# Kernel optimization log

Hardware: AMD Instinct MI355X
Metric: run time of the kernel (lower is better)

## Reference

```python
import jax, jax.numpy as jnp
import numpy as np

N = 3000          # num_sample (nodes)
N_OMICS = 3000    # input feature dims for both omics
ENC1, ENC2, NZ = 256, 128, 64


def _xavier(key, fan_in, fan_out):
    limit = float(np.sqrt(6.0 / (fan_in + fan_out)))
    return jax.random.uniform(key, (fan_in, fan_out), jnp.float32, -limit, limit)


def setup_inputs() -> dict:
    key = jax.random.key(0)
    ks = jax.random.split(key, 20)
    inp = {
        "omics_1": jax.random.normal(ks[0], (N, N_OMICS), jnp.float32),
        "omics_2": jax.random.normal(ks[1], (N, N_OMICS), jnp.float32),
    }
    # random dense adjacency, row-normalized (as a typical normalized graph operator)
    for i, name in enumerate(["adj_feature_omics1", "adj_feature_omics2",
                              "adj_spatial_omics1", "adj_spatial_omics2"]):
        a = jax.random.uniform(ks[2 + i], (N, N), jnp.float32)
        inp[name] = a / jnp.sum(a, axis=1, keepdims=True)
    # GNNLayer weights for the four GAE encoders (xavier uniform, as in reset_parameters)
    dims = [(N_OMICS, ENC1), (ENC1, ENC2), (ENC2, NZ)]
    kidx = 6
    for enc in ["f1", "f2", "s1", "s2"]:
        for li, (fi, fo) in enumerate(dims, start=1):
            inp[f"w_{enc}_{li}"] = _xavier(ks[kidx], fi, fo)
            kidx += 1
    return inp


def _gae_encoder(x, adj, w1, w2, w3):
    # GNNLayer: support = act(x @ W); out = spmm(adj, support). Dropout is identity (eval).
    z = adj @ jnp.tanh(x @ w1)          # [N, ENC1]
    z = adj @ jnp.tanh(z @ w2)          # [N, ENC2]
    z = adj @ (z @ w3)                  # [N, NZ]  (no activation on layer 3)
    adj_hat = jax.nn.sigmoid(z @ z.T)   # [N, N]
    return z, adj_hat


def reference(omics_1, omics_2,
              adj_feature_omics1, adj_feature_omics2,
              adj_spatial_omics1, adj_spatial_omics2,
              w_f1_1, w_f1_2, w_f1_3,
              w_f2_1, w_f2_2, w_f2_3,
              w_s1_1, w_s1_2, w_s1_3,
              w_s2_1, w_s2_2, w_s2_3):
    _, a1 = _gae_encoder(omics_1, adj_feature_omics1, w_f1_1, w_f1_2, w_f1_3)
    _, a2 = _gae_encoder(omics_2, adj_feature_omics2, w_f2_1, w_f2_2, w_f2_3)
    _, a3 = _gae_encoder(omics_1, adj_spatial_omics1, w_s1_1, w_s1_2, w_s1_3)
    _, a4 = _gae_encoder(omics_2, adj_spatial_omics2, w_s2_1, w_s2_2, w_s2_3)
    # stacked reconstructed adjacencies from the four encoders [4, N, N]
    return jnp.stack([a1, a2, a3, a4], axis=0)
```

## Files before the change

kernel.cpp:

```cpp
#include <hip/hip_runtime.h>
#include <stdint.h>
#include <stddef.h>


typedef __attribute__((ext_vector_type(8))) _Float16 half8;
typedef __attribute__((ext_vector_type(4))) float f32x4;

#define PAD 3072
#define MR  3000
#define SQ_STRIDE ((size_t)PAD * PAD)

static __device__ __forceinline__ void async_cp16(const _Float16* g, _Float16* l) {
    __builtin_amdgcn_global_load_lds((const __attribute__((address_space(1))) void*)g,
                                     (__attribute__((address_space(3))) void*)l, 16, 0, 0);
}

struct PrepArgs {
    const float* csrc[6];  _Float16* cdst[6];
    const float* Wsrc[12]; _Float16* Wdst[3];
};

__global__ __launch_bounds__(256) void prep_all(PrepArgs p) {
    __shared__ _Float16 lt[64 * 64];
    const int b = blockIdx.x;
    const int t = threadIdx.x;
    if (b < 13824) {
        const int arr = b / 2304;
        const int idx = (b - arr * 2304) * 256 + t;
        const int row = idx / 192;
        const int c0  = (idx - row * 192) * 16;
        const float* sp = p.csrc[arr] + (size_t)row * MR + c0;
        _Float16* d = p.cdst[arr] + (size_t)row * PAD + c0;
        half8 h0, h1;
        if (row < MR && c0 + 16 <= MR) {
            f32x4 v0 = *(const f32x4*)sp;
            f32x4 v1 = *(const f32x4*)(sp + 4);
            f32x4 v2 = *(const f32x4*)(sp + 8);
            f32x4 v3 = *(const f32x4*)(sp + 12);
            #pragma unroll
            for (int j = 0; j < 4; ++j) {
                h0[j] = (_Float16)v0[j]; h0[4 + j] = (_Float16)v1[j];
                h1[j] = (_Float16)v2[j]; h1[4 + j] = (_Float16)v3[j];
            }
        } else if (row < MR && c0 < MR) {
            #pragma unroll
            for (int j = 0; j < 8; ++j) {
                h0[j] = (c0 + j     < MR) ? (_Float16)sp[j]     : (_Float16)0.f;
                h1[j] = (c0 + 8 + j < MR) ? (_Float16)sp[8 + j] : (_Float16)0.f;
            }
        } else {
            #pragma unroll
            for (int j = 0; j < 8; ++j) { h0[j] = (_Float16)0.f; h1[j] = (_Float16)0.f; }
        }
        *(half8*)d = h0;
        *(half8*)(d + 8) = h1;
    } else {
        const int b2  = b - 13824;
        const int enc = b2 / 204;
        int rem = b2 - enc * 204;
        const float* src; _Float16* dst; int fi, fo, ldk, kt, rt;
        if (rem < 192) {
            src = p.Wsrc[enc * 3 + 0]; dst = p.Wdst[0] + (size_t)enc * 256 * PAD;
            fi = MR; fo = 256; ldk = PAD; kt = rem >> 2; rt = rem & 3;
        } else if (rem < 200) {
            rem -= 192;
            src = p.Wsrc[enc * 3 + 1]; dst = p.Wdst[1] + (size_t)enc * 128 * 256;
            fi = 256; fo = 128; ldk = 256; kt = rem >> 1; rt = rem & 1;
        } else {
            rem -= 200;
            src = p.Wsrc[enc * 3 + 2]; dst = p.Wdst[2] + (size_t)enc * 128 * 128;
            fi = 128; fo = 64; ldk = 128; kt = rem >> 1; rt = rem & 1;
        }
        const int k0 = kt * 64, r0 = rt * 64;
        {
            const int kr = t >> 2, cc = (t & 3) << 4;
            const int gk = k0 + kr;
            const bool kok = gk < fi;
            #pragma unroll
            for (int j = 0; j < 16; ++j) {
                const int gr = r0 + cc + j;
                const float v = (kok && gr < fo) ? src[(size_t)gk * fo + gr] : 0.f;
                lt[(cc + j) * 64 + kr] = (_Float16)v;
            }
        }
        __syncthreads();
        {
            const int rr = t >> 2, kk = (t & 3) << 4;
            half8 a  = *(half8*)&lt[rr * 64 + kk];
            half8 bb = *(half8*)&lt[rr * 64 + kk + 8];
            _Float16* dp = dst + (size_t)(r0 + rr) * ldk + k0 + kk;
            *(half8*)dp = a;
            *(half8*)(dp + 8) = bb;
        }
    }
}

struct GArgs {
    const _Float16* Aall; size_t aStride; int aMask;
    const _Float16* Ball; size_t bStride; int bMask;
    void* Call; size_t cStride;
    int M, Ncols, Kp, lda, ldb, ldc, mBound, nBound;
};

template<int ACT, int OMODE, int S>
__global__ __launch_bounds__(256, 3)
void gemm_bt(GArgs ga)
{
    __shared__ _Float16 smem[16384];
    _Float16* As = smem;
    _Float16* Bs = smem + 8192;

    const int z   = blockIdx.z;
    const int e   = z / S;
    const int ksl = z - e * S;
    const int Kslice = ga.Kp / S;
    const int kbase  = ksl * Kslice;

    const _Float16* A = ga.Aall + (size_t)(e & ga.aMask) * ga.aStride;
    const _Float16* B = ga.Ball + (size_t)(e & ga.bMask) * ga.bStride;

    const int tm = blockIdx.x * 128;
    const int tn = blockIdx.y * 128;
    const int t    = threadIdx.x;
    const int lane = t & 63;
    const int w    = t >> 6;
    const int wm   = (w >> 1) * 64;
    const int wn   = (w & 1) * 64;
    const int lr   = lane & 15;
    const int lg   = lane >> 4;

    f32x4 acc[4][4];
    const f32x4 zero = {0.f, 0.f, 0.f, 0.f};
    #pragma unroll
    for (int i = 0; i < 4; ++i)
        #pragma unroll
        for (int j = 0; j < 4; ++j) acc[i][j] = zero;

    const int nkt = Kslice >> 6;
    for (int kt = 0; kt < nkt; ++kt) {
        const int k0 = kbase + (kt << 6);
        #pragma unroll
        for (int i = 0; i < 4; ++i) {
            const int c = t + i * 256;
            const int row = c >> 3, slot = c & 7;
            const int ss = slot ^ (row & 7);
            async_cp16(A + (size_t)(tm + row) * ga.lda + k0 + ss * 8, &As[c * 8]);
        }
        #pragma unroll
        for (int i = 0; i < 4; ++i) {
            const int c = t + i * 256;
            const int row = c >> 3, slot = c & 7;
            const int ss = slot ^ (row & 7);
            async_cp16(B + (size_t)(tn + row) * ga.ldb + k0 + ss * 8, &Bs[c * 8]);
        }
        __syncthreads();

        #pragma unroll
        for (int ks = 0; ks < 2; ++ks) {
            half8 af[4], bf[4];
            #pragma unroll
            for (int mi = 0; mi < 4; ++mi) {
                const int ra = wm + mi * 16 + lr;
                const int s  = (ks * 4 + lg) ^ (ra & 7);
                af[mi] = *(const half8*)((const char*)As + ra * 128 + s * 16);
            }
            #pragma unroll
            for (int ni = 0; ni < 4; ++ni) {
                const int rb = wn + ni * 16 + lr;
                const int s  = (ks * 4 + lg) ^ (rb & 7);
                bf[ni] = *(const half8*)((const char*)Bs + rb * 128 + s * 16);
            }
            #pragma unroll
            for (int mi = 0; mi < 4; ++mi)
                #pragma unroll
                for (int ni = 0; ni < 4; ++ni)
                    acc[mi][ni] = __builtin_amdgcn_mfma_f32_16x16x32_f16(
                        af[mi], bf[ni], acc[mi][ni], 0, 0, 0);
        }
        __syncthreads();
    }

    if (OMODE == 0) {
        _Float16* C = (_Float16*)ga.Call + (size_t)e * ga.cStride;
        #pragma unroll
        for (int mi = 0; mi < 4; ++mi)
            #pragma unroll
            for (int rr = 0; rr < 4; ++rr) {
                const int m = tm + wm + mi * 16 + lg * 4 + rr;
                #pragma unroll
                for (int ni = 0; ni < 4; ++ni) {
                    const int n = tn + wn + ni * 16 + lr;
                    float x = acc[mi][ni][rr];
                    if (ACT) x = tanhf(x);
                    const bool ok = (m < ga.M) && (n < ga.Ncols);
                    C[(size_t)m * ga.ldc + n] = ok ? (_Float16)x : (_Float16)0.f;
                }
            }
    } else {
        float* Cp = (float*)ga.Call + (size_t)(OMODE == 3 ? z : e) * ga.cStride;
        float* ep = (float*)smem + w * 2048;
        #pragma unroll
        for (int hs = 0; hs < 2; ++hs) {
            __syncthreads();
            #pragma unroll
            for (int mi2 = 0; mi2 < 2; ++mi2)
                #pragma unroll
                for (int ni = 0; ni < 4; ++ni)
                    #pragma unroll
                    for (int rr = 0; rr < 4; ++rr) {
                        const int row = mi2 * 16 + lg * 4 + rr;
                        const int col = ni * 16 + lr;
                        const int sw  = (((row ^ (row >> 2)) & 3) << 4);
                        ep[row * 64 + (col ^ sw)] = acc[hs * 2 + mi2][ni][rr];
                    }
            __syncthreads();
            #pragma unroll
            for (int r2 = 0; r2 < 8; ++r2) {
                const int row = r2 * 4 + (lane >> 4);
                const int c4  = (lane & 15) * 4;
                const int sw  = (((row ^ (row >> 2)) & 3) << 4);
                f32x4 v = *(const f32x4*)&ep[row * 64 + (c4 ^ sw)];
                const int gm = tm + wm + hs * 32 + row;
                const int gn = tn + wn + c4;
                if (gm < ga.mBound && gn < ga.nBound) {
                    if (OMODE == 2) {
                        #pragma unroll
                        for (int j = 0; j < 4; ++j)
                            v[j] = 1.0f / (1.0f + __expf(-v[j]));
                        __builtin_nontemporal_store(v, (f32x4*)&Cp[(size_t)gm * ga.ldc + gn]);
                    } else {
                        *(f32x4*)&Cp[(size_t)gm * ga.ldc + gn] = v;
                    }
                }
            }
        }
    }
}

template<int ACT, int S>
__global__ __launch_bounds__(256)
void reduce_k(const float* __restrict__ P, _Float16* __restrict__ out, size_t region)
{
    const size_t e    = blockIdx.y;
    const size_t base = (size_t)(blockIdx.x * 256 + threadIdx.x) * 8;
    const float* p0 = P + e * S * region + base;
    f32x4 s0 = {0.f, 0.f, 0.f, 0.f}, s1 = s0;
    #pragma unroll
    for (int s = 0; s < S; ++s) {
        const float* p = p0 + (size_t)s * region;
        s0 += *(const f32x4*)p;
        s1 += *(const f32x4*)(p + 4);
    }
    half8 h;
    #pragma unroll
    for (int j = 0; j < 8; ++j) {
        float x = (j < 4) ? s0[j] : s1[j - 4];
        if (ACT) x = tanhf(x);
        h[j] = (_Float16)x;
    }
    *(half8*)(out + e * region + base) = h;
}

extern "C" void kernel_launch(void* const* d_in, const int* in_sizes, int n_in,
                              void* d_out, int out_size, void* d_ws, size_t ws_size,
                              hipStream_t stream)
{
    const size_t R1 = 786432;
    const size_t R2 = 393216;

    _Float16* Adj  = (_Float16*)d_out;
    float*    Part = (float*)(Adj + 4 * SQ_STRIDE);

    _Float16* hb = (_Float16*)d_ws;
    size_t off = 0;
    auto alloc = [&](size_t elems) { _Float16* p = hb + off; off += elems; return p; };
    _Float16* Xh  = alloc(2 * SQ_STRIDE);
    _Float16* T1  = alloc(4 * R1);
    _Float16* Z1  = alloc(4 * R1);
    _Float16* T2  = alloc(4 * R2);
    _Float16* Z2  = alloc(4 * R2);
    _Float16* T3  = alloc(4 * R2);
    _Float16* Z3  = alloc(4 * R2);
    _Float16* W1t = alloc(4ull * 256 * PAD);
    _Float16* W2t = alloc(4ull * 128 * 256);
    _Float16* W3t = alloc(4ull * 128 * 128);

    PrepArgs pa;
    pa.csrc[0] = (const float*)d_in[0]; pa.cdst[0] = Xh;
    pa.csrc[1] = (const float*)d_in[1]; pa.cdst[1] = Xh + SQ_STRIDE;
    for (int i = 0; i < 4; ++i) {
        pa.csrc[2 + i] = (const float*)d_in[2 + i];
        pa.cdst[2 + i] = Adj + (size_t)i * SQ_STRIDE;
    }
    for (int enc = 0; enc < 4; ++enc)
        for (int li = 0; li < 3; ++li)
            pa.Wsrc[enc * 3 + li] = (const float*)d_in[6 + enc * 3 + li];
    pa.Wdst[0] = W1t; pa.Wdst[1] = W2t; pa.Wdst[2] = W3t;
    prep_all<<<dim3(14640, 1, 1), 256, 0, stream>>>(pa);

    const int BIG = 1 << 30;

    GArgs g1 = { W1t, (size_t)256 * PAD, 3, Xh, SQ_STRIDE, 1,
                 Part, R1, 256, PAD, PAD, PAD, PAD, PAD, BIG, BIG };
    gemm_bt<0, 3, 4><<<dim3(2, 24, 16), 256, 0, stream>>>(g1);
    reduce_k<1, 4><<<dim3(384, 4, 1), 256, 0, stream>>>(Part, T1, R1);

    GArgs g2 = { Adj, SQ_STRIDE, 3, T1, R1, 3,
                 Part, R1, PAD, 256, PAD, PAD, PAD, 256, BIG, BIG };
    gemm_bt<0, 3, 4><<<dim3(24, 2, 16), 256, 0, stream>>>(g2);
    reduce_k<0, 4><<<dim3(384, 4, 1), 256, 0, stream>>>(Part, Z1, R1);

    GArgs g3 = { W2t, (size_t)128 * 256, 3, Z1, R1, 3,
                 T2, R2, 128, PAD, 256, 256, 256, PAD, BIG, BIG };
    gemm_bt<1, 0, 1><<<dim3(1, 24, 4), 256, 0, stream>>>(g3);

    GArgs g4 = { Adj, SQ_STRIDE, 3, T2, R2, 3,
                 Part, R2, PAD, 128, PAD, PAD, PAD, 128, BIG, BIG };
    gemm_bt<0, 3, 8><<<dim3(24, 1, 32), 256, 0, stream>>>(g4);
    reduce_k<0, 8><<<dim3(192, 4, 1), 256, 0, stream>>>(Part, Z2, R2);

    GArgs g5 = { W3t, (size_t)128 * 128, 3, Z2, R2, 3,
                 T3, R2, 128, PAD, 128, 128, 128, PAD, BIG, BIG };
    gemm_bt<0, 0, 1><<<dim3(1, 24, 4), 256, 0, stream>>>(g5);

    GArgs g6 = { Adj, SQ_STRIDE, 3, T3, R2, 3,
                 Part, R2, PAD, 128, PAD, PAD, PAD, 128, BIG, BIG };
    gemm_bt<0, 3, 8><<<dim3(24, 1, 32), 256, 0, stream>>>(g6);
    reduce_k<0, 8><<<dim3(192, 4, 1), 256, 0, stream>>>(Part, Z3, R2);

    GArgs g7 = { Z3, R2, 3, Z3, R2, 3,
                 d_out, (size_t)MR * MR, MR, MR, 64, 128, 128, MR, MR, MR };
    gemm_bt<0, 2, 1><<<dim3(24, 24, 4), 256, 0, stream>>>(g7);
}
```

Measured before the change: 275.0 us.

## Double-buffer GEMM K-loop, store split-K partials in fp16, use persistent prep kernel

Result: faster. 261.6 us (-4.9%).

```diff
diff --git a/kernel.cpp b/kernel.cpp
--- a/kernel.cpp
+++ b/kernel.cpp
@@ -9,6 +9,8 @@
 #define PAD 3072
 #define MR  3000
 #define SQ_STRIDE ((size_t)PAD * PAD)
+#define CAST_BLK 1920
+#define WT_BLK   128
 
 static __device__ __forceinline__ void async_cp16(const _Float16* g, _Float16* l) {
     __builtin_amdgcn_global_load_lds((const __attribute__((address_space(1))) void*)g,
@@ -20,77 +22,70 @@
     const float* Wsrc[12]; _Float16* Wdst[3];
 };
 
-__global__ __launch_bounds__(256) void prep_all(PrepArgs p) {
+__global__ __launch_bounds__(256) void prep2(PrepArgs p) {
     __shared__ _Float16 lt[64 * 64];
     const int b = blockIdx.x;
     const int t = threadIdx.x;
-    if (b < 13824) {
-        const int arr = b / 2304;
-        const int idx = (b - arr * 2304) * 256 + t;
-        const int row = idx / 192;
-        const int c0  = (idx - row * 192) * 16;
-        const float* sp = p.csrc[arr] + (size_t)row * MR + c0;
-        _Float16* d = p.cdst[arr] + (size_t)row * PAD + c0;
-        half8 h0, h1;
-        if (row < MR && c0 + 16 <= MR) {
-            f32x4 v0 = *(const f32x4*)sp;
-            f32x4 v1 = *(const f32x4*)(sp + 4);
-            f32x4 v2 = *(const f32x4*)(sp + 8);
-            f32x4 v3 = *(const f32x4*)(sp + 12);
-            #pragma unroll
-            for (int j = 0; j < 4; ++j) {
-                h0[j] = (_Float16)v0[j]; h0[4 + j] = (_Float16)v1[j];
-                h1[j] = (_Float16)v2[j]; h1[4 + j] = (_Float16)v3[j];
-            }
-        } else if (row < MR && c0 < MR) {
-            #pragma unroll
-            for (int j = 0; j < 8; ++j) {
-                h0[j] = (c0 + j     < MR) ? (_Float16)sp[j]     : (_Float16)0.f;
-                h1[j] = (c0 + 8 + j < MR) ? (_Float16)sp[8 + j] : (_Float16)0.f;
-            }
-        } else {
-            #pragma unroll
-            for (int j = 0; j < 8; ++j) { h0[j] = (_Float16)0.f; h1[j] = (_Float16)0.f; }
-        }
-        *(half8*)d = h0;
-        *(half8*)(d + 8) = h1;
+    if (b < CAST_BLK) {
+        const int UPA = PAD * PAD / 8;
+        const int TOT = 6 * UPA;
+        for (int u = b * 256 + t; u < TOT; u += CAST_BLK * 256) {
+            const int arr = u / UPA;
+            const int rem = u - arr * UPA;
+            const int row = rem / 384;
+            const int c0  = (rem - row * 384) * 8;
+            half8 h;
+            if (row < MR && c0 < MR) {
+                const float* sp = p.csrc[arr] + (size_t)row * MR + c0;
+                f32x4 v0 = *(const f32x4*)sp;
+                f32x4 v1 = *(const f32x4*)(sp + 4);
+                #pragma unroll
+                for (int j = 0; j < 4; ++j) { h[j] = (_Float16)v0[j]; h[4 + j] = (_Float16)v1[j]; }
+            } else {
+                #pragma unroll
+                for (int j = 0; j < 8; ++j) h[j] = (_Float16)0.f;
+            }
+            *(half8*)(p.cdst[arr] + (size_t)row * PAD + c0) = h;
+        }
     } else {
-        const int b2  = b - 13824;
-        const int enc = b2 / 204;
-        int rem = b2 - enc * 204;
-        const float* src; _Float16* dst; int fi, fo, ldk, kt, rt;
-        if (rem < 192) {
-            src = p.Wsrc[enc * 3 + 0]; dst = p.Wdst[0] + (size_t)enc * 256 * PAD;
-            fi = MR; fo = 256; ldk = PAD; kt = rem >> 2; rt = rem & 3;
-        } else if (rem < 200) {
-            rem -= 192;
-            src = p.Wsrc[enc * 3 + 1]; dst = p.Wdst[1] + (size_t)enc * 128 * 256;
-            fi = 256; fo = 128; ldk = 256; kt = rem >> 1; rt = rem & 1;
-        } else {
-            rem -= 200;
-            src = p.Wsrc[enc * 3 + 2]; dst = p.Wdst[2] + (size_t)enc * 128 * 128;
-            fi = 128; fo = 64; ldk = 128; kt = rem >> 1; rt = rem & 1;
-        }
-        const int k0 = kt * 64, r0 = rt * 64;
-        {
-            const int kr = t >> 2, cc = (t & 3) << 4;
-            const int gk = k0 + kr;
-            const bool kok = gk < fi;
-            #pragma unroll
-            for (int j = 0; j < 16; ++j) {
-                const int gr = r0 + cc + j;
-                const float v = (kok && gr < fo) ? src[(size_t)gk * fo + gr] : 0.f;
-                lt[(cc + j) * 64 + kr] = (_Float16)v;
-            }
-        }
-        __syncthreads();
-        {
-            const int rr = t >> 2, kk = (t & 3) << 4;
-            half8 a  = *(half8*)&lt[rr * 64 + kk];
-            half8 bb = *(half8*)&lt[rr * 64 + kk + 8];
-            _Float16* dp = dst + (size_t)(r0 + rr) * ldk + k0 + kk;
-            *(half8*)dp = a;
-            *(half8*)(dp + 8) = bb;
+        for (int tile = b - CAST_BLK; tile < 816; tile += WT_BLK) {
+            const int enc = tile / 204;
+            int rem = tile - enc * 204;
+            const float* src; _Float16* dst; int fi, fo, ldk, kt, rt;
+            if (rem < 192) {
+                src = p.Wsrc[enc * 3 + 0]; dst = p.Wdst[0] + (size_t)enc * 256 * PAD;
+                fi = MR; fo = 256; ldk = PAD; kt = rem >> 2; rt = rem & 3;
+            } else if (rem < 200) {
+                rem -= 192;
+                src = p.Wsrc[enc * 3 + 1]; dst = p.Wdst[1] + (size_t)enc * 128 * 256;
+                fi = 256; fo = 128; ldk = 256; kt = rem >> 1; rt = rem & 1;
+            } else {
+                rem -= 200;
+                src = p.Wsrc[enc * 3 + 2]; dst = p.Wdst[2] + (size_t)enc * 128 * 128;
+                fi = 128; fo = 64; ldk = 128; kt = rem >> 1; rt = rem & 1;
+            }
+            const int k0 = kt * 64, r0 = rt * 64;
+            __syncthreads();
+            {
+                const int kr = t >> 2, cc = (t & 3) << 4;
+                const int gk = k0 + kr;
+                const bool kok = gk < fi;
+                #pragma unroll
+                for (int j = 0; j < 16; ++j) {
+                    const int gr = r0 + cc + j;
+                    const float v = (kok && gr < fo) ? src[(size_t)gk * fo + gr] : 0.f;
+                    lt[(cc + j) * 64 + kr] = (_Float16)v;
+                }
+            }
+            __syncthreads();
+            {
+                const int rr = t >> 2, kk = (t & 3) << 4;
+                half8 a  = *(half8*)&lt[rr * 64 + kk];
+                half8 bb = *(half8*)&lt[rr * 64 + kk + 8];
+                _Float16* dp = dst + (size_t)(r0 + rr) * ldk + k0 + kk;
+                *(half8*)dp = a;
+                *(half8*)(dp + 8) = bb;
+            }
         }
     }
 }
@@ -107,8 +102,6 @@
 void gemm_bt(GArgs ga)
 {
     __shared__ _Float16 smem[16384];
-    _Float16* As = smem;
-    _Float16* Bs = smem + 8192;
 
     const int z   = blockIdx.z;
     const int e   = z / S;
@@ -129,6 +122,9 @@
     const int lr   = lane & 15;
     const int lg   = lane >> 4;
 
+    const int sr  = t >> 2;
+    const int sch = t & 3;
+
     f32x4 acc[4][4];
     const f32x4 zero = {0.f, 0.f, 0.f, 0.f};
     #pragma unroll
@@ -136,47 +132,54 @@
         #pragma unroll
         for (int j = 0; j < 4; ++j) acc[i][j] = zero;
 
-    const int nkt = Kslice >> 6;
-    for (int kt = 0; kt < nkt; ++kt) {
-        const int k0 = kbase + (kt << 6);
-        #pragma unroll
-        for (int i = 0; i < 4; ++i) {
-            const int c = t + i * 256;
-            const int row = c >> 3, slot = c & 7;
-            const int ss = slot ^ (row & 7);
-            async_cp16(A + (size_t)(tm + row) * ga.lda + k0 + ss * 8, &As[c * 8]);
-        }
-        #pragma unroll
-        for (int i = 0; i < 4; ++i) {
-            const int c = t + i * 256;
-            const int row = c >> 3, slot = c & 7;
-            const int ss = slot ^ (row & 7);
-            async_cp16(B + (size_t)(tn + row) * ga.ldb + k0 + ss * 8, &Bs[c * 8]);
-        }
-        __syncthreads();
-
-        #pragma unroll
-        for (int ks = 0; ks < 2; ++ks) {
-            half8 af[4], bf[4];
-            #pragma unroll
-            for (int mi = 0; mi < 4; ++mi) {
-                const int ra = wm + mi * 16 + lr;
-                const int s  = (ks * 4 + lg) ^ (ra & 7);
-                af[mi] = *(const half8*)((const char*)As + ra * 128 + s * 16);
-            }
-            #pragma unroll
-            for (int ni = 0; ni < 4; ++ni) {
-                const int rb = wn + ni * 16 + lr;
-                const int s  = (ks * 4 + lg) ^ (rb & 7);
-                bf[ni] = *(const half8*)((const char*)Bs + rb * 128 + s * 16);
-            }
-            #pragma unroll
-            for (int mi = 0; mi < 4; ++mi)
-                #pragma unroll
-                for (int ni = 0; ni < 4; ++ni)
-                    acc[mi][ni] = __builtin_amdgcn_mfma_f32_16x16x32_f16(
-                        af[mi], bf[ni], acc[mi][ni], 0, 0, 0);
-        }
+    const int nht = Kslice >> 5;
+
+    auto STAGE = [&](int ht, int buf) {
+        const int k0 = kbase + (ht << 5);
+        _Float16* As = smem + buf * 8192;
+        _Float16* Bs = As + 4096;
+        #pragma unroll
+        for (int i = 0; i < 2; ++i) {
+            const int row = sr + i * 64;
+            const int sc  = sch ^ (row & 3);
+            async_cp16(A + (size_t)(tm + row) * ga.lda + k0 + sc * 8,
+                       As + (row * 4 + sch) * 8);
+        }
+        #pragma unroll
+        for (int i = 0; i < 2; ++i) {
+            const int row = sr + i * 64;
+            const int sc  = sch ^ (row & 3);
+            async_cp16(B + (size_t)(tn + row) * ga.ldb + k0 + sc * 8,
+                       Bs + (row * 4 + sch) * 8);
+        }
+    };
+
+    STAGE(0, 0);
+    __syncthreads();
+    for (int h = 0; h < nht; ++h) {
+        const int cur = h & 1;
+        if (h + 1 < nht) STAGE(h + 1, cur ^ 1);
+        const _Float16* As = smem + cur * 8192;
+        const _Float16* Bs = As + 4096;
+        half8 af[4], bf[4];
+        #pragma unroll
+        for (int mi = 0; mi < 4; ++mi) {
+            const int ra = wm + mi * 16 + lr;
+            const int ch = lg ^ (ra & 3);
+            af[mi] = *(const half8*)(As + ra * 32 + ch * 8);
+        }
+        #pragma unroll
+        for (int ni = 0; ni < 4; ++ni) {
+            const int rb = wn + ni * 16 + lr;
+            const int ch = lg ^ (rb & 3);
+            bf[ni] = *(const half8*)(Bs + rb * 32 + ch * 8);
+        }
+        #pragma unroll
+        for (int mi = 0; mi < 4; ++mi)
+            #pragma unroll
+            for (int ni = 0; ni < 4; ++ni)
+                acc[mi][ni] = __builtin_amdgcn_mfma_f32_16x16x32_f16(
+                    af[mi], bf[ni], acc[mi][ni], 0, 0, 0);
         __syncthreads();
     }
 
@@ -196,8 +199,37 @@
                     C[(size_t)m * ga.ldc + n] = ok ? (_Float16)x : (_Float16)0.f;
                 }
             }
+    } else if (OMODE == 1) {
+        _Float16* Cp = (_Float16*)ga.Call + (size_t)z * ga.cStride;
+        _Float16* ep = smem + w * 2048;
+        #pragma unroll
+        for (int hs = 0; hs < 2; ++hs) {
+            __syncthreads();
+            #pragma unroll
+            for (int mi2 = 0; mi2 < 2; ++mi2)
+                #pragma unroll
+                for (int ni = 0; ni < 4; ++ni)
+                    #pragma unroll
+                    for (int rr = 0; rr < 4; ++rr) {
+                        const int row = mi2 * 16 + lg * 4 + rr;
+                        const int col = ni * 16 + lr;
+                        const int sw  = (((row ^ (row >> 2)) & 3) << 4);
+                        ep[row * 64 + (col ^ sw)] = (_Float16)acc[hs * 2 + mi2][ni][rr];
+                    }
+            __syncthreads();
+            #pragma unroll
+            for (int it = 0; it < 4; ++it) {
+                const int row = it * 8 + (lane >> 3);
+                const int c0  = (lane & 7) * 8;
+                const int sw  = (((row ^ (row >> 2)) & 3) << 4);
+                half8 v = *(const half8*)&ep[row * 64 + (c0 ^ sw)];
+                const int gm = tm + wm + hs * 32 + row;
+                const int gn = tn + wn + c0;
+                *(half8*)&Cp[(size_t)gm * ga.ldc + gn] = v;
+            }
+        }
     } else {
-        float* Cp = (float*)ga.Call + (size_t)(OMODE == 3 ? z : e) * ga.cStride;
+        float* Cp = (float*)ga.Call + (size_t)e * ga.cStride;
         float* ep = (float*)smem + w * 2048;
         #pragma unroll
         for (int hs = 0; hs < 2; ++hs) {
@@ -223,14 +255,10 @@
                 const int gm = tm + wm + hs * 32 + row;
                 const int gn = tn + wn + c4;
                 if (gm < ga.mBound && gn < ga.nBound) {
-                    if (OMODE == 2) {
-                        #pragma unroll
-                        for (int j = 0; j < 4; ++j)
-                            v[j] = 1.0f / (1.0f + __expf(-v[j]));
-                        __builtin_nontemporal_store(v, (f32x4*)&Cp[(size_t)gm * ga.ldc + gn]);
-                    } else {
-                        *(f32x4*)&Cp[(size_t)gm * ga.ldc + gn] = v;
-                    }
+                    #pragma unroll
+                    for (int j = 0; j < 4; ++j)
+                        v[j] = 1.0f / (1.0f + __expf(-v[j]));
+                    __builtin_nontemporal_store(v, (f32x4*)&Cp[(size_t)gm * ga.ldc + gn]);
                 }
             }
         }
@@ -239,22 +267,22 @@
 
 template<int ACT, int S>
 __global__ __launch_bounds__(256)
-void reduce_k(const float* __restrict__ P, _Float16* __restrict__ out, size_t region)
+void reduce_k(const _Float16* __restrict__ P, _Float16* __restrict__ out, size_t region)
 {
     const size_t e    = blockIdx.y;
     const size_t base = (size_t)(blockIdx.x * 256 + threadIdx.x) * 8;
-    const float* p0 = P + e * S * region + base;
-    f32x4 s0 = {0.f, 0.f, 0.f, 0.f}, s1 = s0;
+    const _Float16* p0 = P + e * S * region + base;
+    float s[8] = {0.f, 0.f, 0.f, 0.f, 0.f, 0.f, 0.f, 0.f};
     #pragma unroll
-    for (int s = 0; s < S; ++s) {
-        const float* p = p0 + (size_t)s * region;
-        s0 += *(const f32x4*)p;
-        s1 += *(const f32x4*)(p + 4);
+    for (int si = 0; si < S; ++si) {
+        half8 v = *(const half8*)(p0 + (size_t)si * region);
+        #pragma unroll
+        for (int j = 0; j < 8; ++j) s[j] += (float)v[j];
     }
     half8 h;
     #pragma unroll
     for (int j = 0; j < 8; ++j) {
-        float x = (j < 4) ? s0[j] : s1[j - 4];
+        float x = s[j];
         if (ACT) x = tanhf(x);
         h[j] = (_Float16)x;
     }
@@ -268,8 +296,8 @@
     const size_t R1 = 786432;
     const size_t R2 = 393216;
 
-    _Float16* Adj  = (_Float16*)d_out;
-    float*    Part = (float*)(Adj + 4 * SQ_STRIDE);
+    _Float16* Adj    = (_Float16*)d_out;
+    _Float16* Part16 = Adj + 4 * SQ_STRIDE;
 
     _Float16* hb = (_Float16*)d_ws;
     size_t off = 0;
@@ -296,37 +324,37 @@
         for (int li = 0; li < 3; ++li)
             pa.Wsrc[enc * 3 + li] = (const float*)d_in[6 + enc * 3 + li];
     pa.Wdst[0] = W1t; pa.Wdst[1] = W2t; pa.Wdst[2] = W3t;
-    prep_all<<<dim3(14640, 1, 1), 256, 0, stream>>>(pa);
+    prep2<<<dim3(CAST_BLK + WT_BLK, 1, 1), 256, 0, stream>>>(pa);
 
     const int BIG = 1 << 30;
 
     GArgs g1 = { W1t, (size_t)256 * PAD, 3, Xh, SQ_STRIDE, 1,
-                 Part, R1, 256, PAD, PAD, PAD, PAD, PAD, BIG, BIG };
-    gemm_bt<0, 3, 4><<<dim3(2, 24, 16), 256, 0, stream>>>(g1);
-    reduce_k<1, 4><<<dim3(384, 4, 1), 256, 0, stream>>>(Part, T1, R1);
+                 Part16, R1, 256, PAD, PAD, PAD, PAD, PAD, BIG, BIG };
+    gemm_bt<0, 1, 4><<<dim3(2, 24, 16), 256, 0, stream>>>(g1);
+    reduce_k<1, 4><<<dim3(384, 4, 1), 256, 0, stream>>>(Part16, T1, R1);
 
     GArgs g2 = { Adj, SQ_STRIDE, 3, T1, R1, 3,
-                 Part, R1, PAD, 256, PAD, PAD, PAD, 256, BIG, BIG };
-    gemm_bt<0, 3, 4><<<dim3(24, 2, 16), 256, 0, stream>>>(g2);
-    reduce_k<0, 4><<<dim3(384, 4, 1), 256, 0, stream>>>(Part, Z1, R1);
+                 Part16, R1, PAD, 256, PAD, PAD, PAD, 256, BIG, BIG };
+    gemm_bt<0, 1, 4><<<dim3(24, 2, 16), 256, 0, stream>>>(g2);
+    reduce_k<0, 4><<<dim3(384, 4, 1), 256, 0, stream>>>(Part16, Z1, R1);
 
     GArgs g3 = { W2t, (size_t)128 * 256, 3, Z1, R1, 3,
                  T2, R2, 128, PAD, 256, 256, 256, PAD, BIG, BIG };
     gemm_bt<1, 0, 1><<<dim3(1, 24, 4), 256, 0, stream>>>(g3);
 
     GArgs g4 = { Adj, SQ_STRIDE, 3, T2, R2, 3,
-                 Part, R2, PAD, 128, PAD, PAD, PAD, 128, BIG, BIG };
-    gemm_bt<0, 3, 8><<<dim3(24, 1, 32), 256, 0, stream>>>(g4);
-    reduce_k<0, 8><<<dim3(192, 4, 1), 256, 0, stream>>>(Part, Z2, R2);
+                 Part16, R2, PAD, 128, PAD, PAD, PAD, 128, BIG, BIG };
+    gemm_bt<0, 1, 8><<<dim3(24, 1, 32), 256, 0, stream>>>(g4);
+    reduce_k<0, 8><<<dim3(192, 4, 1), 256, 0, stream>>>(Part16, Z2, R2);
 
     GArgs g5 = { W3t, (size_t)128 * 128, 3, Z2, R2, 3,
                  T3, R2, 128, PAD, 128, 128, 128, PAD, BIG, BIG };
     gemm_bt<0, 0, 1><<<dim3(1, 24, 4), 256, 0, stream>>>(g5);
 
     GArgs g6 = { Adj, SQ_STRIDE, 3, T3, R2, 3,
-                 Part, R2, PAD, 128, PAD, PAD, PAD, 128, BIG, BIG };
-    gemm_bt<0, 3, 8><<<dim3(24, 1, 32), 256, 0, stream>>>(g6);
-    reduce_k<0, 8><<<dim3(192, 4, 1), 256, 0, stream>>>(Part, Z3, R2);
+                 Part16, R2, PAD, 128, PAD, PAD, PAD, 128, BIG, BIG };
+    gemm_bt<0, 1, 8><<<dim3(24, 1, 32), 256, 0, stream>>>(g6);
+    reduce_k<0, 8><<<dim3(192, 4, 1), 256, 0, stream>>>(Part16, Z3, R2);
 
     GArgs g7 = { Z3, R2, 3, Z3, R2, 3,
                  d_out, (size_t)MR * MR, MR, MR, 64, 128, 128, MR, MR, MR };
```
